# Kernel tuning notes

Measured on AMD Instinct MI355X. Metric: run time of the kernel, lower is better.

## Reference

```python
import jax, jax.numpy as jnp
import numpy as np

DIM = 2048
N_HEADS = 16
KV_LORA = 512
NOPE = 128
ROPE = 64
V_DIM = 128
QK_DIM = NOPE + ROPE  # 192
B, S = 2, 2048
ROPE_THETA = 10000.0
ROPE_FACTOR = 40.0
BETA_FAST, BETA_SLOW = 32, 1
ORIG_LEN, MAX_LEN = 4096, 16384
MSCALE_ARG = 1.0
EPS = 1e-6


def _precompute_freqs(seqlen):
    # DeepSeek YaRN-corrected rotary frequencies (interleaved-pair convention).
    d = ROPE
    freqs = 1.0 / (ROPE_THETA ** (np.arange(0, d, 2, dtype=np.float64) / d))
    if MAX_LEN > ORIG_LEN:
        def corr_dim(n_rot):
            return d * np.log(ORIG_LEN / (n_rot * 2 * np.pi)) / (2 * np.log(ROPE_THETA))
        low = max(int(np.floor(corr_dim(BETA_FAST))), 0)
        high = min(int(np.ceil(corr_dim(BETA_SLOW))), d - 1)
        smooth = 1.0 - np.clip((np.arange(d // 2) - low) / max(high - low, 1e-3), 0, 1)
        freqs = freqs / ROPE_FACTOR * (1 - smooth) + freqs * smooth
    t = np.arange(seqlen, dtype=np.float64)
    ang = np.outer(t, freqs)  # [S, d/2]
    return np.cos(ang).astype(np.float32), np.sin(ang).astype(np.float32)


def softmax_scale():
    scale = QK_DIM ** -0.5
    if MAX_LEN > ORIG_LEN:
        m = 0.1 * MSCALE_ARG * float(np.log(ROPE_FACTOR)) + 1.0
        scale = scale * m * m
    return scale


def setup_inputs() -> dict:
    key = jax.random.key(0)
    ks = jax.random.split(key, 6)
    w_std = 0.02
    fc, fs = _precompute_freqs(S)
    return {
        "x": jax.random.normal(ks[0], (B, S, DIM), jnp.float32),
        "wq": jax.random.normal(ks[1], (N_HEADS * QK_DIM, DIM), jnp.float32) * w_std,
        "wkv_a": jax.random.normal(ks[2], (KV_LORA + ROPE, DIM), jnp.float32) * w_std,
        "kv_norm_w": jnp.ones((KV_LORA,), jnp.float32),
        "wkv_b": jax.random.normal(ks[3], (N_HEADS * (NOPE + V_DIM), KV_LORA), jnp.float32) * w_std,
        "wo": jax.random.normal(ks[4], (DIM, N_HEADS * V_DIM), jnp.float32) * w_std,
        "freqs_cos": jnp.asarray(fc),
        "freqs_sin": jnp.asarray(fs),
    }


def _apply_rotary(x, cos, sin):
    # x: [B, S, H, d]; interleaved complex pairs, cos/sin: [S, d/2]
    xr = x.reshape(*x.shape[:-1], -1, 2)
    x_re, x_im = xr[..., 0], xr[..., 1]
    c = cos[None, :, None, :]
    s = sin[None, :, None, :]
    y_re = x_re * c - x_im * s
    y_im = x_re * s + x_im * c
    return jnp.stack((y_re, y_im), axis=-1).reshape(x.shape)


def _rmsnorm(x, w):
    return x * jax.lax.rsqrt(jnp.mean(x * x, axis=-1, keepdims=True) + EPS) * w


def reference(x, wq, wkv_a, kv_norm_w, wkv_b, wo, freqs_cos, freqs_sin):
    b, s, _ = x.shape
    # Q projection (q_lora_rank == 0 path)
    q = (x @ wq.T).reshape(b, s, N_HEADS, QK_DIM)
    q_nope, q_pe = q[..., :NOPE], q[..., NOPE:]
    q_pe = _apply_rotary(q_pe, freqs_cos, freqs_sin)
    # Low-rank KV compression
    kv = x @ wkv_a.T  # [B, S, 512+64]
    kv_c, k_pe = kv[..., :KV_LORA], kv[..., KV_LORA:]
    k_pe = _apply_rotary(k_pe[:, :, None, :], freqs_cos, freqs_sin)  # [B,S,1,64]
    kv_c = _rmsnorm(kv_c, kv_norm_w)
    kvb = (kv_c @ wkv_b.T).reshape(b, s, N_HEADS, NOPE + V_DIM)
    k_nope, v = kvb[..., :NOPE], kvb[..., NOPE:]
    k = jnp.concatenate([k_nope, jnp.broadcast_to(k_pe, (b, s, N_HEADS, ROPE))], axis=-1)
    # Causal attention
    scores = jnp.einsum("bshd,bthd->bhst", q, k) * softmax_scale()
    causal = jnp.tril(jnp.ones((s, s), bool))
    scores = jnp.where(causal[None, None], scores, jnp.float32(-1e30))
    p = jax.nn.softmax(scores, axis=-1)
    out = jnp.einsum("bhst,bthd->bshd", p, v).reshape(b, s, N_HEADS * V_DIM)
    return out @ wo.T
```

## Files before the change

### kernel.cpp

```cpp
#include <hip/hip_runtime.h>
#include <math.h>

#define NH      16
#define D_NOPE  128
#define D_ROPE  64
#define D_QK    192
#define D_V     128
#define KV_LORA 512
#define NB      2
#define SEQ     2048
#define NTOK    (NB*SEQ)
#define QROW    (NH*D_QK)
#define KVBROW  (NH*(D_NOPE+D_V))
#define EPSF    1e-6f

typedef unsigned short u16;
typedef float  floatx4 __attribute__((ext_vector_type(4)));
typedef __bf16 bf16x8  __attribute__((ext_vector_type(8)));
typedef u16    u16x4   __attribute__((ext_vector_type(4)));
typedef u16    u16x8   __attribute__((ext_vector_type(8)));

__device__ __forceinline__ u16 f2bf(float f) {
    unsigned u = __builtin_bit_cast(unsigned, f);
    return (u16)((u + 0x7fffu + ((u >> 16) & 1u)) >> 16);
}

__device__ __forceinline__ void async_copy16(const void* g, void* l) {
    __builtin_amdgcn_global_load_lds(
        (const __attribute__((address_space(1))) unsigned int*)g,
        (__attribute__((address_space(3))) unsigned int*)l,
        16, 0, 0);
}

__global__ __launch_bounds__(256) void cast_all(const float* __restrict__ x,
                                                const float* __restrict__ wq,
                                                const float* __restrict__ wkva,
                                                const float* __restrict__ wkvb,
                                                const float* __restrict__ wo,
                                                u16* __restrict__ xb,
                                                u16* __restrict__ wqb,
                                                u16* __restrict__ wkvab,
                                                u16* __restrict__ wkvbb,
                                                u16* __restrict__ wob) {
    int blk = blockIdx.x;
    const float* src; u16* dst; bool pad = false;
    if (blk < 8192)        { src = x;    dst = xb; }
    else if (blk < 14336)  { blk -= 8192;  src = wq;   dst = wqb; }
    else if (blk < 15616)  { blk -= 14336; src = wkva; dst = wkvab; pad = true; }
    else if (blk < 17664)  { blk -= 15616; src = wkvb; dst = wkvbb; }
    else                   { blk -= 17664; src = wo;   dst = wob; }
    const int i = (blk * 256 + threadIdx.x) * 4;
    u16x4 o;
    if (pad && (i >> 11) >= 576) {
        o[0] = 0; o[1] = 0; o[2] = 0; o[3] = 0;
    } else {
        const float4 v = *(const float4*)&src[i];
        o[0] = f2bf(v.x); o[1] = f2bf(v.y); o[2] = f2bf(v.z); o[3] = f2bf(v.w);
    }
    *(u16x4*)&dst[i] = o;
}

template<int MODE>
__global__ __launch_bounds__(256) void gemm_mfma(const u16* __restrict__ A,
                                                 const u16* __restrict__ B,
                                                 void* __restrict__ Cout,
                                                 u16* __restrict__ kbuf,
                                                 u16* __restrict__ vT,
                                                 int M, int N, int K) {
    __shared__ u16 As[128 * 32];
    __shared__ u16 Bs[128 * 32];
    const int tid  = threadIdx.x;
    const int wave = tid >> 6, lane = tid & 63;
    const int m0 = blockIdx.y * 128, n0 = blockIdx.x * 128;
    const int wm = (wave & 1) * 64, wn = (wave >> 1) * 64;

    const int srow = wave * 32 + (lane >> 2);
    const int kch  = (lane & 3) * 8;
    const u16* gA0 = A + (size_t)(m0 + srow) * K + kch;
    const u16* gA1 = gA0 + (size_t)16 * K;
    const u16* gB0 = B + (size_t)(n0 + srow) * K + kch;
    const u16* gB1 = gB0 + (size_t)16 * K;
    u16* lA0 = &As[(wave * 32) * 32];
    u16* lA1 = &As[(wave * 32 + 16) * 32];
    u16* lB0 = &Bs[(wave * 32) * 32];
    u16* lB1 = &Bs[(wave * 32 + 16) * 32];

    floatx4 acc[4][4];
#pragma unroll
    for (int i = 0; i < 4; ++i)
#pragma unroll
        for (int j = 0; j < 4; ++j) acc[i][j] = 0.f;

    const int lrow = lane & 15;
    const int lkh  = (lane >> 4) * 8;

    for (int k0 = 0; k0 < K; k0 += 32) {
        __syncthreads();
        async_copy16(gA0 + k0, lA0);
        async_copy16(gA1 + k0, lA1);
        async_copy16(gB0 + k0, lB0);
        async_copy16(gB1 + k0, lB1);
        __syncthreads();
        bf16x8 a[4], b[4];
#pragma unroll
        for (int mi = 0; mi < 4; ++mi)
            a[mi] = *(const bf16x8*)&As[(wm + mi * 16 + lrow) * 32 + lkh];
#pragma unroll
        for (int ni = 0; ni < 4; ++ni)
            b[ni] = *(const bf16x8*)&Bs[(wn + ni * 16 + lrow) * 32 + lkh];
#pragma unroll
        for (int mi = 0; mi < 4; ++mi)
#pragma unroll
            for (int ni = 0; ni < 4; ++ni)
                acc[mi][ni] = __builtin_amdgcn_mfma_f32_16x16x32_bf16(
                    a[mi], b[ni], acc[mi][ni], 0, 0, 0);
    }

    const int crow = (lane >> 4) * 4, ccol = lane & 15;
#pragma unroll
    for (int mi = 0; mi < 4; ++mi)
#pragma unroll
        for (int ni = 0; ni < 4; ++ni) {
            const int m = m0 + wm + mi * 16 + crow;
            const int c = n0 + wn + ni * 16 + ccol;
            if (MODE == 0) {
                float* cp = (float*)Cout + (size_t)m * N + c;
#pragma unroll
                for (int r = 0; r < 4; ++r) cp[(size_t)r * N] = acc[mi][ni][r];
            } else if (MODE == 1) {
                u16* cp = (u16*)Cout + (size_t)m * N + c;
#pragma unroll
                for (int r = 0; r < 4; ++r) cp[(size_t)r * N] = f2bf(acc[mi][ni][r]);
            } else {
                const int hh = c >> 8, j = c & 255;
                const int bb = m >> 11, t = m & 2047;
                if (j < 128) {
#pragma unroll
                    for (int r = 0; r < 4; ++r)
                        kbuf[(((size_t)hh * 2 + bb) * 2048 + t + r) * 192 + j] =
                            f2bf(acc[mi][ni][r]);
                } else {
                    u16x4 pk;
#pragma unroll
                    for (int r = 0; r < 4; ++r) pk[r] = f2bf(acc[mi][ni][r]);
                    *(u16x4*)&vT[(((size_t)hh * 2 + bb) * 128 + (j - 128)) * 2048 + t] = pk;
                }
            }
        }
}


__global__ __launch_bounds__(256) void kv_fix(const float* __restrict__ kv_raw,
                                              const float* __restrict__ w,
                                              const float* __restrict__ fcos,
                                              const float* __restrict__ fsin,
                                              u16* __restrict__ kvn_bf,
                                              u16* __restrict__ kbuf) {
    const int row = blockIdx.x;
    const int tid = threadIdx.x;
    const float* src = kv_raw + (size_t)row * 640;
    const float v0 = src[tid];
    const float v1 = src[256 + tid];
    float ss = v0 * v0 + v1 * v1;
#pragma unroll
    for (int off = 32; off > 0; off >>= 1) ss += __shfl_down(ss, off, 64);
    __shared__ float red[4];
    __shared__ float kpe_s[64];
    if ((tid & 63) == 0) red[tid >> 6] = ss;
    if (tid < 32) {
        const int s = row & (SEQ - 1);
        const float c  = fcos[s * 32 + tid];
        const float sn = fsin[s * 32 + tid];
        const float xr = src[KV_LORA + 2 * tid];
        const float xi = src[KV_LORA + 2 * tid + 1];
        kpe_s[2 * tid]     = xr * c - xi * sn;
        kpe_s[2 * tid + 1] = xr * sn + xi * c;
    }
    __syncthreads();
    const float tot = red[0] + red[1] + red[2] + red[3];
    const float inv = rsqrtf(tot * (1.0f / KV_LORA) + EPSF);
    kvn_bf[(size_t)row * KV_LORA + tid]       = f2bf(v0 * inv * w[tid]);
    kvn_bf[(size_t)row * KV_LORA + 256 + tid] = f2bf(v1 * inv * w[256 + tid]);
    const int bb = row >> 11, t = row & 2047;
    const int hh = tid >> 4, dg = (tid & 15) * 4;
    u16x4 pk;
#pragma unroll
    for (int j = 0; j < 4; ++j) pk[j] = f2bf(kpe_s[dg + j]);
    *(u16x4*)&kbuf[(((size_t)hh * 2 + bb) * 2048 + t) * 192 + 128 + dg] = pk;
}

__global__ __launch_bounds__(256, 2) void attn_mfma(const u16* __restrict__ qbf,
                                                    const u16* __restrict__ kbuf,
                                                    const u16* __restrict__ vT,
                                                    u16* __restrict__ att,
                                                    float scale) {
    __shared__ __attribute__((aligned(16))) u16 Ks[2][6 * 64 * 32];
    __shared__ __attribute__((aligned(16))) u16 Vs[2 * 128 * 32];
    __shared__ __attribute__((aligned(16))) u16 Ps[4][16 * 72];
    const int x = blockIdx.x;
    const int qt_base = (x & 1) ? (15 - (x >> 1)) : (x >> 1);
    const int qt = blockIdx.z ? (15 - qt_base) : qt_base;
    const int h = blockIdx.y, b = blockIdx.z;
    const int tid = threadIdx.x, wave = tid >> 6, lane = tid & 63;
    const int l15 = lane & 15, lg = lane >> 4;

    const u16* kb_base = kbuf + ((size_t)(h * 2 + b)) * 2048 * 192;
    const u16* vt_base = vT   + ((size_t)(h * 2 + b)) * 128 * 2048;

    int qrow[2];
    bf16x8 qf[2][6];
#pragma unroll
    for (int g = 0; g < 2; ++g) {
        qrow[g] = qt * 128 + g * 64 + wave * 16 + l15;
        const size_t qoff = ((size_t)(b * SEQ + qrow[g])) * QROW + h * 192 + lg * 8;
#pragma unroll
        for (int s = 0; s < 6; ++s) qf[g][s] = *(const bf16x8*)&qbf[qoff + s * 32];
    }

    floatx4 oacc[2][8];
#pragma unroll
    for (int g = 0; g < 2; ++g)
#pragma unroll
        for (int v = 0; v < 8; ++v) oacc[g][v] = 0.f;
    float m_run[2] = {-1e30f, -1e30f}, l_run[2] = {0.f, 0.f};

    auto stageK = [&](int bufi, int tt) {
#pragma unroll
        for (int i = 0; i < 6; ++i) {
            const int base = (wave * 6 + i) * 64;
            const int slot = base + lane;
            const int s = slot >> 8, r = slot & 255, tk = r >> 2, ch = r & 3;
            async_copy16(kb_base + ((size_t)(tt + tk)) * 192 + s * 32 + ch * 8,
                         &Ks[bufi][base * 8]);
        }
    };
    auto stageV = [&](int tt) {
#pragma unroll
        for (int i = 0; i < 4; ++i) {
            const int base = (wave * 4 + i) * 64;
            const int slot = base + lane;
            const int s = slot >> 9, r = slot & 511, v = r >> 2, ch = r & 3;
            async_copy16(vt_base + ((size_t)v) * 2048 + tt + s * 32 + ch * 8,
                         &Vs[base * 8]);
        }
    };

    const int kt_max = 2 * qt + 1;
    stageK(0, 0);
    __syncthreads();

    for (int kt = 0; kt <= kt_max; ++kt) {
        const int t0 = kt * 64;
        const int cur = kt & 1;

        stageV(t0);
        if (kt < kt_max) stageK(cur ^ 1, t0 + 64);

        floatx4 sacc[2][4];
#pragma unroll
        for (int g = 0; g < 2; ++g)
#pragma unroll
            for (int mt = 0; mt < 4; ++mt) sacc[g][mt] = 0.f;
        __builtin_amdgcn_s_setprio(1);
#pragma unroll
        for (int s = 0; s < 6; ++s) {
#pragma unroll
            for (int mt = 0; mt < 4; ++mt) {
                const bf16x8 kf = *(const bf16x8*)&Ks[cur][(s * 64 + mt * 16 + l15) * 32 + lg * 8];
#pragma unroll
                for (int g = 0; g < 2; ++g)
                    sacc[g][mt] = __builtin_amdgcn_mfma_f32_16x16x32_bf16(
                        kf, qf[g][s], sacc[g][mt], 0, 0, 0);
            }
        }
        __builtin_amdgcn_s_setprio(0);

        u16x4 pk[2][4];
#pragma unroll
        for (int g = 0; g < 2; ++g) {
            const bool full = (t0 + 63) <= (qt * 128 + g * 64 + wave * 16);
            float p[16];
            float tmax = -1e30f;
#pragma unroll
            for (int mt = 0; mt < 4; ++mt)
#pragma unroll
                for (int r = 0; r < 4; ++r) {
                    float v = sacc[g][mt][r] * scale;
                    if (!full) {
                        const int tglob = t0 + mt * 16 + lg * 4 + r;
                        v = (tglob <= qrow[g]) ? v : -1e30f;
                    }
                    p[mt * 4 + r] = v;
                    tmax = fmaxf(tmax, v);
                }
            tmax = fmaxf(tmax, __shfl_xor(tmax, 16));
            tmax = fmaxf(tmax, __shfl_xor(tmax, 32));
            const bool defer = __all(tmax <= m_run[g] + 8.0f);
            float alph = 1.0f;
            float mnew = m_run[g];
            if (!defer) {
                mnew = fmaxf(m_run[g], tmax);
                alph = __expf(m_run[g] - mnew);
                m_run[g] = mnew;
            }
            float rsum = 0.f;
#pragma unroll
            for (int k = 0; k < 16; ++k) { p[k] = __expf(p[k] - mnew); rsum += p[k]; }
            rsum += __shfl_xor(rsum, 16);
            rsum += __shfl_xor(rsum, 32);
            if (!defer) {
                l_run[g] = l_run[g] * alph + rsum;
                float af[4];
#pragma unroll
                for (int r = 0; r < 4; ++r) af[r] = __shfl(alph, lg * 4 + r);
#pragma unroll
                for (int vt = 0; vt < 8; ++vt)
#pragma unroll
                    for (int r = 0; r < 4; ++r) oacc[g][vt][r] *= af[r];
            } else {
                l_run[g] += rsum;
            }
#pragma unroll
            for (int mt = 0; mt < 4; ++mt)
#pragma unroll
                for (int r = 0; r < 4; ++r) pk[g][mt][r] = f2bf(p[mt * 4 + r]);
        }

        __syncthreads();

        __builtin_amdgcn_s_setprio(1);
#pragma unroll
        for (int g = 0; g < 2; ++g) {
#pragma unroll
            for (int mt = 0; mt < 4; ++mt)
                *(u16x4*)&Ps[wave][l15 * 72 + mt * 16 + lg * 4] = pk[g][mt];
            bf16x8 pf[2];
#pragma unroll
            for (int s = 0; s < 2; ++s)
                pf[s] = *(const bf16x8*)&Ps[wave][l15 * 72 + s * 32 + lg * 8];
#pragma unroll
            for (int s = 0; s < 2; ++s)
#pragma unroll
                for (int vt = 0; vt < 8; ++vt) {
                    const bf16x8 vf = *(const bf16x8*)&Vs[(s * 128 + vt * 16 + l15) * 32 + lg * 8];
                    oacc[g][vt] = __builtin_amdgcn_mfma_f32_16x16x32_bf16(
                        pf[s], vf, oacc[g][vt], 0, 0, 0);
                }
        }
        __builtin_amdgcn_s_setprio(0);

        __syncthreads();
    }
#pragma unroll
    for (int g = 0; g < 2; ++g) {
        float lf[4];
#pragma unroll
        for (int r = 0; r < 4; ++r) lf[r] = 1.0f / __shfl(l_run[g], lg * 4 + r);
#pragma unroll
        for (int vt = 0; vt < 8; ++vt)
#pragma unroll
            for (int r = 0; r < 4; ++r) {
                const int orow = b * SEQ + qt * 128 + g * 64 + wave * 16 + lg * 4 + r;
                att[(size_t)orow * 2048 + h * 128 + vt * 16 + l15] =
                    f2bf(oacc[g][vt][r] * lf[r]);
            }
    }
}

extern "C" void kernel_launch(void* const* d_in, const int* in_sizes, int n_in,
                              void* d_out, int out_size, void* d_ws, size_t ws_size,
                              hipStream_t stream) {
    const float* x     = (const float*)d_in[0];
    const float* wq    = (const float*)d_in[1];
    const float* wkv_a = (const float*)d_in[2];
    const float* knw   = (const float*)d_in[3];
    const float* wkv_b = (const float*)d_in[4];
    const float* wo    = (const float*)d_in[5];
    const float* fcos  = (const float*)d_in[6];
    const float* fsin  = (const float*)d_in[7];
    float* out = (float*)d_out;

    char* w = (char*)d_ws;
    u16*   x_bf    = (u16*)w;  w += (size_t)NTOK * 2048 * 2;
    u16*   wq_bf   = (u16*)w;  w += (size_t)QROW * 2048 * 2;
    u16*   wkva_bf = (u16*)w;  w += (size_t)640 * 2048 * 2;
    u16*   wkvb_bf = (u16*)w;  w += (size_t)KVBROW * KV_LORA * 2;
    u16*   wo_bf   = (u16*)w;  w += (size_t)2048 * 2048 * 2;
    u16*   q_bf    = (u16*)w;  w += (size_t)NTOK * QROW * 2;
    float* kv_raw  = (float*)w; w += (size_t)NTOK * 640 * 4;
    u16*   kvn_bf  = (u16*)w;  w += (size_t)NTOK * KV_LORA * 2;
    u16*   kbuf    = (u16*)w;  w += (size_t)NH * NB * SEQ * 192 * 2;
    u16*   vT      = (u16*)w;  w += (size_t)NH * NB * 128 * SEQ * 2;
    u16*   att_bf  = (u16*)w;  w += (size_t)NTOK * 2048 * 2;

    const double mm = 0.1 * 1.0 * log(40.0) + 1.0;
    const float scale = (float)((1.0 / sqrt((double)D_QK)) * mm * mm);

    dim3 blk(256);
    cast_all<<<dim3(21760), blk, 0, stream>>>(x, wq, wkv_a, wkv_b, wo,
                                              x_bf, wq_bf, wkva_bf, wkvb_bf, wo_bf);
    gemm_mfma<1><<<dim3(QROW / 128, NTOK / 128), blk, 0, stream>>>(
        x_bf, wq_bf, q_bf, nullptr, nullptr, NTOK, QROW, 2048);
    gemm_mfma<0><<<dim3(640 / 128, NTOK / 128), blk, 0, stream>>>(
        x_bf, wkva_bf, kv_raw, nullptr, nullptr, NTOK, 640, 2048);
    kv_fix<<<dim3(NTOK), blk, 0, stream>>>(kv_raw, knw, fcos, fsin, kvn_bf, kbuf);
    gemm_mfma<2><<<dim3(KVBROW / 128, NTOK / 128), blk, 0, stream>>>(
        kvn_bf, wkvb_bf, nullptr, kbuf, vT, NTOK, KVBROW, KV_LORA);
    attn_mfma<<<dim3(SEQ / 128, NH, NB), blk, 0, stream>>>(q_bf, kbuf, vT, att_bf, scale);
    gemm_mfma<0><<<dim3(2048 / 128, NTOK / 128), blk, 0, stream>>>(
        att_bf, wo_bf, out, nullptr, nullptr, NTOK, 2048, 2048);
}
```

Baseline: 441.1 us.

## Swizzle K/V LDS tiles and use partial vmcnt waits with raw barriers

Applies an XOR swizzle to the 16-byte chunk index when staging K and V tiles into LDS, and matches it on the MFMA fragment reads, to cut LDS bank conflicts. Replaces the full __syncthreads with explicit s_waitcnt vmcnt counts plus s_barrier, so V loads and next-K prefetches can stay in flight while the QK and softmax stages run. The PV loop is reorganised so each V fragment feeds both row groups. The hand-tuned vmcnt counts depend on exactly how many async copies are outstanding, which makes the code fragile if the staging changes.

```diff
diff --git a/kernel.cpp b/kernel.cpp
--- a/kernel.cpp
+++ b/kernel.cpp
@@ -203,6 +203,7 @@
     const int h = blockIdx.y, b = blockIdx.z;
     const int tid = threadIdx.x, wave = tid >> 6, lane = tid & 63;
     const int l15 = lane & 15, lg = lane >> 4;
+    const int lgs = lg ^ ((l15 >> 1) & 3);
 
     const u16* kb_base = kbuf + ((size_t)(h * 2 + b)) * 2048 * 192;
     const u16* vt_base = vT   + ((size_t)(h * 2 + b)) * 128 * 2048;
@@ -230,7 +231,8 @@
             const int base = (wave * 6 + i) * 64;
             const int slot = base + lane;
             const int s = slot >> 8, r = slot & 255, tk = r >> 2, ch = r & 3;
-            async_copy16(kb_base + ((size_t)(tt + tk)) * 192 + s * 32 + ch * 8,
+            const int chs = ch ^ ((tk >> 1) & 3);
+            async_copy16(kb_base + ((size_t)(tt + tk)) * 192 + s * 32 + chs * 8,
                          &Ks[bufi][base * 8]);
         }
     };
@@ -240,21 +242,27 @@
             const int base = (wave * 4 + i) * 64;
             const int slot = base + lane;
             const int s = slot >> 9, r = slot & 511, v = r >> 2, ch = r & 3;
-            async_copy16(vt_base + ((size_t)v) * 2048 + tt + s * 32 + ch * 8,
+            const int chs = ch ^ ((v >> 1) & 3);
+            async_copy16(vt_base + ((size_t)v) * 2048 + tt + s * 32 + chs * 8,
                          &Vs[base * 8]);
         }
     };
 
     const int kt_max = 2 * qt + 1;
     stageK(0, 0);
-    __syncthreads();
 
     for (int kt = 0; kt <= kt_max; ++kt) {
         const int t0 = kt * 64;
         const int cur = kt & 1;
 
         stageV(t0);
-        if (kt < kt_max) stageK(cur ^ 1, t0 + 64);
+        if (kt < kt_max) {
+            stageK(cur ^ 1, t0 + 64);
+            asm volatile("s_waitcnt vmcnt(10)" ::: "memory");
+        } else {
+            asm volatile("s_waitcnt vmcnt(4)" ::: "memory");
+        }
+        __builtin_amdgcn_s_barrier();
 
         floatx4 sacc[2][4];
 #pragma unroll
@@ -266,7 +274,7 @@
         for (int s = 0; s < 6; ++s) {
 #pragma unroll
             for (int mt = 0; mt < 4; ++mt) {
-                const bf16x8 kf = *(const bf16x8*)&Ks[cur][(s * 64 + mt * 16 + l15) * 32 + lg * 8];
+                const bf16x8 kf = *(const bf16x8*)&Ks[cur][(s * 64 + mt * 16 + l15) * 32 + lgs * 8];
 #pragma unroll
                 for (int g = 0; g < 2; ++g)
                     sacc[g][mt] = __builtin_amdgcn_mfma_f32_16x16x32_bf16(
@@ -326,30 +334,35 @@
                 for (int r = 0; r < 4; ++r) pk[g][mt][r] = f2bf(p[mt * 4 + r]);
         }
 
-        __syncthreads();
-
-        __builtin_amdgcn_s_setprio(1);
+        bf16x8 pf[2][2];
 #pragma unroll
         for (int g = 0; g < 2; ++g) {
 #pragma unroll
             for (int mt = 0; mt < 4; ++mt)
                 *(u16x4*)&Ps[wave][l15 * 72 + mt * 16 + lg * 4] = pk[g][mt];
-            bf16x8 pf[2];
 #pragma unroll
             for (int s = 0; s < 2; ++s)
-                pf[s] = *(const bf16x8*)&Ps[wave][l15 * 72 + s * 32 + lg * 8];
-#pragma unroll
-            for (int s = 0; s < 2; ++s)
-#pragma unroll
-                for (int vt = 0; vt < 8; ++vt) {
-                    const bf16x8 vf = *(const bf16x8*)&Vs[(s * 128 + vt * 16 + l15) * 32 + lg * 8];
-                    oacc[g][vt] = __builtin_amdgcn_mfma_f32_16x16x32_bf16(
-                        pf[s], vf, oacc[g][vt], 0, 0, 0);
-                }
-        }
+                pf[g][s] = *(const bf16x8*)&Ps[wave][l15 * 72 + s * 32 + lg * 8];
+        }
+
+        if (kt < kt_max) asm volatile("s_waitcnt vmcnt(6)" ::: "memory");
+        else             asm volatile("s_waitcnt vmcnt(0)" ::: "memory");
+        __builtin_amdgcn_s_barrier();
+
+        __builtin_amdgcn_s_setprio(1);
+#pragma unroll
+        for (int s = 0; s < 2; ++s)
+#pragma unroll
+            for (int vt = 0; vt < 8; ++vt) {
+                const bf16x8 vf = *(const bf16x8*)&Vs[(s * 128 + vt * 16 + l15) * 32 + lgs * 8];
+                oacc[0][vt] = __builtin_amdgcn_mfma_f32_16x16x32_bf16(
+                    pf[0][s], vf, oacc[0][vt], 0, 0, 0);
+                oacc[1][vt] = __builtin_amdgcn_mfma_f32_16x16x32_bf16(
+                    pf[1][s], vf, oacc[1][vt], 0, 0, 0);
+            }
         __builtin_amdgcn_s_setprio(0);
 
-        __syncthreads();
+        __builtin_amdgcn_s_barrier();
     }
 #pragma unroll
     for (int g = 0; g < 2; ++g) {
```

Measured after the change: 432.4 us. -2.0%, faster.
